# Kernel tuning notes

Hardware: AMD Instinct MI355X
Metric: run time of the kernel (lower is better)

Reference implementation:

```python
import jax, jax.numpy as jnp
import numpy as np

B, S, D, H = 64, 512, 256, 512

def setup_inputs() -> dict:
    key = jax.random.key(0)
    ks = jax.random.split(key, 16)
    s_in = 1.0 / np.sqrt(D)
    s_h = 1.0 / np.sqrt(H)
    inp = {
        "inputs": jax.random.normal(ks[0], (B, S, D), jnp.float32),
        # input-side gate weights (stored [D,H], equiv to torch Linear weight.T)
        "Wf": jax.random.uniform(ks[1], (D, H), jnp.float32, -s_in, s_in),
        "Wi": jax.random.uniform(ks[2], (D, H), jnp.float32, -s_in, s_in),
        "Wo": jax.random.uniform(ks[3], (D, H), jnp.float32, -s_in, s_in),
        "Wc": jax.random.uniform(ks[4], (D, H), jnp.float32, -s_in, s_in),
        "bf": jax.random.uniform(ks[5], (H,), jnp.float32, -s_in, s_in),
        "bi": jax.random.uniform(ks[6], (H,), jnp.float32, -s_in, s_in),
        "bo": jax.random.uniform(ks[7], (H,), jnp.float32, -s_in, s_in),
        "bc": jax.random.uniform(ks[8], (H,), jnp.float32, -s_in, s_in),
        # recurrent weights (bias=False)
        "Uf": jax.random.uniform(ks[9], (H, H), jnp.float32, -s_h, s_h),
        "Ui": jax.random.uniform(ks[10], (H, H), jnp.float32, -s_h, s_h),
        "Uo": jax.random.uniform(ks[11], (H, H), jnp.float32, -s_h, s_h),
        "Uc": jax.random.uniform(ks[12], (H, H), jnp.float32, -s_h, s_h),
        # output head
        "Wfc": jax.random.uniform(ks[13], (H, 1), jnp.float32, -s_h, s_h),
        "bfc": jax.random.uniform(ks[14], (1,), jnp.float32, -s_h, s_h),
    }
    return inp


def reference(inputs, Wf, Wi, Wo, Wc, bf, bi, bo, bc, Uf, Ui, Uo, Uc, Wfc, bfc):
    # Precompute all input-side gate projections in one big GEMM: [B,S,4H]
    Wx = jnp.concatenate([Wf, Wi, Wo, Wc], axis=1)            # [D,4H]
    bx = jnp.concatenate([bf, bi, bo, bc], axis=0)            # [4H]
    gx = jnp.einsum('bsd,dg->bsg', inputs, Wx) + bx           # [B,S,4H]
    Uh = jnp.concatenate([Uf, Ui, Uo, Uc], axis=1)            # [H,4H]

    h0 = jnp.zeros((inputs.shape[0], Uf.shape[0]), inputs.dtype)
    c0 = jnp.zeros_like(h0)
    Hd = Uf.shape[0]

    def step(carry, gx_t):
        h, c = carry
        g = gx_t + h @ Uh                                     # [B,4H]
        f_t = jax.nn.sigmoid(g[:, 0 * Hd:1 * Hd])
        i_t = jax.nn.sigmoid(g[:, 1 * Hd:2 * Hd])
        o_t = jax.nn.sigmoid(g[:, 2 * Hd:3 * Hd])
        chat = jnp.tanh(g[:, 3 * Hd:4 * Hd])
        c = f_t * c + i_t * chat
        h = o_t * jnp.tanh(c)
        return (h, c), h

    (h_t, c_t), hs = jax.lax.scan(step, (h0, c0), jnp.swapaxes(gx, 0, 1))
    outputs = jnp.swapaxes(hs, 0, 1)                          # [B,S,H]
    predictions = jnp.einsum('bsh,ho->bso', outputs, Wfc) + bfc
    return predictions, h_t, c_t
```

## Files before the change

### kernel.cpp

```cpp
#include <hip/hip_runtime.h>
#include <hip/hip_bf16.h>

#define B_ 64
#define S_ 512
#define D_ 256
#define H_ 512

typedef __attribute__((ext_vector_type(8))) short bf16x8;
typedef __attribute__((ext_vector_type(4))) float f32x4;
typedef __attribute__((ext_vector_type(4))) unsigned int uint4v;
typedef unsigned short ushort_t;

__device__ __forceinline__ ushort_t f2bf(float f) {
    __hip_bfloat16 h = __float2bfloat16(f);
    return *reinterpret_cast<ushort_t*>(&h);
}
__device__ __forceinline__ float sigmoid_f(float x) { return 1.f / (1.f + __expf(-x)); }
__device__ __forceinline__ float tanh_f(float x) { return 1.f - 2.f / (__expf(2.f * x) + 1.f); }

__device__ __forceinline__ void lds_barrier() {
    asm volatile("s_waitcnt lgkmcnt(0)\n\ts_barrier" ::: "memory");
}

__global__ __launch_bounds__(512, 2) void lstm_rec(
    const float* __restrict__ X,
    const float* __restrict__ Wf, const float* __restrict__ Wi,
    const float* __restrict__ Wo, const float* __restrict__ Wc,
    const float* __restrict__ bfp, const float* __restrict__ bip,
    const float* __restrict__ bop, const float* __restrict__ bcp,
    const float* __restrict__ Uf, const float* __restrict__ Ui,
    const float* __restrict__ Uo, const float* __restrict__ Uc,
    const float* __restrict__ Wfc,
    float* __restrict__ pred, unsigned int* __restrict__ hbufU,
    unsigned int* __restrict__ flags, unsigned int* __restrict__ xcdtab,
    float* __restrict__ outH, float* __restrict__ outC)
{
    __shared__ ushort_t hS[16 * 520];
    __shared__ ushort_t xS[16 * 264];
    __shared__ float gact[4][16][68];
    __shared__ int meta[2];

    const int tid  = threadIdx.x;
    const int w    = tid >> 6;
    const int lane = tid & 63;
    const int q    = lane >> 4;
    const int m    = lane & 15;
    const int gate = w >> 1;
    const int half = w & 1;

    if (w == 0) {
        unsigned int xcd;
        asm volatile("s_getreg_b32 %0, hwreg(HW_REG_XCC_ID)" : "=s"(xcd));
        xcd &= 15u;
        if (lane == 0)
            __hip_atomic_store(&xcdtab[blockIdx.x], xcd + 1u,
                               __ATOMIC_RELEASE, __HIP_MEMORY_SCOPE_AGENT);
        unsigned int entry;
        for (;;) {
            entry = __hip_atomic_load(&xcdtab[lane], __ATOMIC_ACQUIRE, __HIP_MEMORY_SCOPE_AGENT);
            if (__ballot(entry != 0u) == ~0ull) break;
            __builtin_amdgcn_s_sleep(1);
        }
        const unsigned int xcd_j = entry - 1u;
        const unsigned int key_j = (xcd_j << 8) | (unsigned int)lane;
        const unsigned int mykey = (xcd << 8) | (unsigned int)blockIdx.x;
        const int rank = __popcll(__ballot(key_j < mykey));
        const int c_lt = __popcll(__ballot(xcd_j < xcd));
        const int c_eq = __popcll(__ballot(xcd_j == xcd));
        const int gg   = rank >> 3;
        const bool uni = (c_lt <= gg * 8) && (gg * 8 + 8 <= c_lt + c_eq);
        if (lane == 0) { meta[0] = rank; meta[1] = uni ? 1 : 0; }
    }
    __syncthreads();
    const int  rank    = meta[0];
    const bool uniform = meta[1] != 0;
    if (rank >= 32) return;
    const int g = rank >> 3;
    const int s = rank & 7;

    const int ncol0 = s * 64 + half * 32 + m;
    const int ncol1 = ncol0 + 16;

    const float* Ug = (gate == 0) ? Uf : (gate == 1) ? Ui : (gate == 2) ? Uo : Uc;
    const float* Wg = (gate == 0) ? Wf : (gate == 1) ? Wi : (gate == 2) ? Wo : Wc;
    const float* bg = (gate == 0) ? bfp : (gate == 1) ? bip : (gate == 2) ? bop : bcp;

    const float bias0 = bg[ncol0];
    const float bias1 = bg[ncol1];

    bf16x8 UF[2][16];
    bf16x8 WF[2][8];
    #pragma unroll
    for (int tt = 0; tt < 2; ++tt) {
        const int nc = tt ? ncol1 : ncol0;
        #pragma unroll
        for (int ks = 0; ks < 16; ++ks) {
            bf16x8 v;
            #pragma unroll
            for (int j = 0; j < 8; ++j)
                v[j] = (short)f2bf(Ug[(ks * 32 + q * 8 + j) * H_ + nc]);
            UF[tt][ks] = v;
        }
        #pragma unroll
        for (int ks = 0; ks < 8; ++ks) {
            bf16x8 v;
            #pragma unroll
            for (int j = 0; j < 8; ++j)
                v[j] = (short)f2bf(Wg[(ks * 32 + q * 8 + j) * H_ + nc]);
            WF[tt][ks] = v;
        }
    }

    const int urow  = tid >> 5;
    const int upair = tid & 31;
    const float2 wfc2 = *(const float2*)&Wfc[s * 64 + 2 * upair];

    float cr0 = 0.f, cr1 = 0.f;

    unsigned int* flagsG = flags + g * 64;
    const int myflag = s * 8 + w;

    {
        const float* xsrc = &X[((size_t)(g * 16 + urow) * S_ + 0) * D_ + upair * 8];
        float4 a = *(const float4*)xsrc;
        float4 b = *(const float4*)(xsrc + 4);
        bf16x8 v;
        v[0] = (short)f2bf(a.x); v[1] = (short)f2bf(a.y);
        v[2] = (short)f2bf(a.z); v[3] = (short)f2bf(a.w);
        v[4] = (short)f2bf(b.x); v[5] = (short)f2bf(b.y);
        v[6] = (short)f2bf(b.z); v[7] = (short)f2bf(b.w);
        *(bf16x8*)&xS[urow * 264 + upair * 8] = v;
    }

    float4 xr0, xr1;

    for (int t = 0; t < S_; ++t) {
        if (t > 0) {
            const unsigned int tgt = (unsigned int)t;
            for (;;) {
                unsigned int f = __hip_atomic_load(&flagsG[lane],
                                                   __ATOMIC_RELAXED, __HIP_MEMORY_SCOPE_AGENT);
                if (__ballot(f >= tgt) == ~0ull) break;
                __builtin_amdgcn_s_sleep(1);
            }
        }

        {
            const int row  = tid >> 5;
            const int dcol = (tid & 31) * 8;
            const unsigned int* p0 = &hbufU[(size_t)((t % 3) * B_ + g * 16 + row) * 256 + dcol];
            const unsigned int* p1 = p0 + 4;
            uint4v ra, rb;
            if (uniform) {
                asm volatile(
                    "global_load_dwordx4 %0, %2, off sc0\n\t"
                    "global_load_dwordx4 %1, %3, off sc0\n\t"
                    "s_waitcnt vmcnt(0)"
                    : "=v"(ra), "=v"(rb) : "v"(p0), "v"(p1) : "memory");
            } else {
                asm volatile(
                    "global_load_dwordx4 %0, %2, off sc0 sc1\n\t"
                    "global_load_dwordx4 %1, %3, off sc0 sc1\n\t"
                    "s_waitcnt vmcnt(0)"
                    : "=v"(ra), "=v"(rb) : "v"(p0), "v"(p1) : "memory");
            }
            *(uint4v*)&hS[row * 520 + dcol * 2]     = ra;
            *(uint4v*)&hS[row * 520 + dcol * 2 + 8] = rb;
        }
        if (t + 1 < S_) {
            const float* xsrc = &X[((size_t)(g * 16 + urow) * S_ + (t + 1)) * D_ + upair * 8];
            xr0 = *(const float4*)xsrc;
            xr1 = *(const float4*)(xsrc + 4);
        }
        lds_barrier();

        f32x4 accA0 = {bias0, bias0, bias0, bias0};
        f32x4 accA1 = {bias1, bias1, bias1, bias1};
        f32x4 accB0 = {0.f, 0.f, 0.f, 0.f};
        f32x4 accB1 = {0.f, 0.f, 0.f, 0.f};
        #pragma unroll
        for (int ks = 0; ks < 8; ++ks) {
            bf16x8 a = *(const bf16x8*)&xS[m * 264 + ks * 32 + q * 8];
            accA0 = __builtin_amdgcn_mfma_f32_16x16x32_bf16(a, WF[0][ks], accA0, 0, 0, 0);
            accA1 = __builtin_amdgcn_mfma_f32_16x16x32_bf16(a, WF[1][ks], accA1, 0, 0, 0);
        }
        #pragma unroll
        for (int ks = 0; ks < 16; ++ks) {
            bf16x8 a = *(const bf16x8*)&hS[m * 520 + ks * 32 + q * 8];
            accB0 = __builtin_amdgcn_mfma_f32_16x16x32_bf16(a, UF[0][ks], accB0, 0, 0, 0);
            accB1 = __builtin_amdgcn_mfma_f32_16x16x32_bf16(a, UF[1][ks], accB1, 0, 0, 0);
        }
        #pragma unroll
        for (int j = 0; j < 4; ++j) {
            float v0 = accA0[j] + accB0[j];
            float v1 = accA1[j] + accB1[j];
            v0 = (gate < 3) ? sigmoid_f(v0) : tanh_f(v0);
            v1 = (gate < 3) ? sigmoid_f(v1) : tanh_f(v1);
            gact[gate][q * 4 + j][half * 32 + m]      = v0;
            gact[gate][q * 4 + j][half * 32 + 16 + m] = v1;
        }
        lds_barrier();

        float2 f2v = *(const float2*)&gact[0][urow][2 * upair];
        float2 i2v = *(const float2*)&gact[1][urow][2 * upair];
        float2 o2v = *(const float2*)&gact[2][urow][2 * upair];
        float2 ch2 = *(const float2*)&gact[3][urow][2 * upair];
        cr0 = f2v.x * cr0 + i2v.x * ch2.x;
        cr1 = f2v.y * cr1 + i2v.y * ch2.y;
        float hv0 = o2v.x * tanh_f(cr0);
        float hv1 = o2v.y * tanh_f(cr1);

        float pv = hv0 * wfc2.x + hv1 * wfc2.y;

        if (t < S_ - 1) {
            unsigned int packed = (unsigned int)f2bf(hv0) | ((unsigned int)f2bf(hv1) << 16);
            unsigned int* hdst =
                &hbufU[(size_t)(((t + 1) % 3) * B_ + g * 16 + urow) * 256 + s * 32 + upair];
            if (uniform) {
                asm volatile("global_store_dword %0, %1, off sc0" :: "v"(hdst), "v"(packed) : "memory");
            } else {
                asm volatile("global_store_dword %0, %1, off sc0 sc1" :: "v"(hdst), "v"(packed) : "memory");
            }
            bf16x8 v;
            v[0] = (short)f2bf(xr0.x); v[1] = (short)f2bf(xr0.y);
            v[2] = (short)f2bf(xr0.z); v[3] = (short)f2bf(xr0.w);
            v[4] = (short)f2bf(xr1.x); v[5] = (short)f2bf(xr1.y);
            v[6] = (short)f2bf(xr1.z); v[7] = (short)f2bf(xr1.w);
            *(bf16x8*)&xS[urow * 264 + upair * 8] = v;

            asm volatile("s_waitcnt vmcnt(0)" ::: "memory");
            if (lane == 0) {
                __hip_atomic_store(&flagsG[myflag], (unsigned int)(t + 1),
                                   __ATOMIC_RELAXED, __HIP_MEMORY_SCOPE_AGENT);
            }
        } else {
            *(float2*)&outH[(g * 16 + urow) * H_ + s * 64 + 2 * upair] = make_float2(hv0, hv1);
            *(float2*)&outC[(g * 16 + urow) * H_ + s * 64 + 2 * upair] = make_float2(cr0, cr1);
        }

        pv += __shfl_xor(pv, 16);
        pv += __shfl_xor(pv, 8);
        pv += __shfl_xor(pv, 4);
        pv += __shfl_xor(pv, 2);
        pv += __shfl_xor(pv, 1);
        if (upair == 0) atomicAdd(&pred[(g * 16 + urow) * S_ + t], pv);
    }
}

__global__ void pred_fin(const float* __restrict__ pred,
                         const float* __restrict__ bfc,
                         float* __restrict__ out)
{
    int i = blockIdx.x * blockDim.x + threadIdx.x;
    if (i < B_ * S_) out[i] = pred[i] + bfc[0];
}

extern "C" void kernel_launch(void* const* d_in, const int* in_sizes, int n_in,
                              void* d_out, int out_size, void* d_ws, size_t ws_size,
                              hipStream_t stream) {
    const float* X   = (const float*)d_in[0];
    const float* Wf  = (const float*)d_in[1];
    const float* Wi  = (const float*)d_in[2];
    const float* Wo  = (const float*)d_in[3];
    const float* Wc  = (const float*)d_in[4];
    const float* bfp = (const float*)d_in[5];
    const float* bip = (const float*)d_in[6];
    const float* bop = (const float*)d_in[7];
    const float* bcp = (const float*)d_in[8];
    const float* Uf  = (const float*)d_in[9];
    const float* Ui  = (const float*)d_in[10];
    const float* Uo  = (const float*)d_in[11];
    const float* Uc  = (const float*)d_in[12];
    const float* Wfc = (const float*)d_in[13];
    const float* bfc = (const float*)d_in[14];

    float*        pred   = (float*)d_ws;
    unsigned int* hbufU  = (unsigned int*)((char*)d_ws + 131072);
    unsigned int* flags  = (unsigned int*)((char*)d_ws + 327680);
    unsigned int* xcdtab = (unsigned int*)((char*)d_ws + 328704);

    hipMemsetAsync(d_ws, 0, 328704 + 256, stream);

    float* out = (float*)d_out;
    lstm_rec<<<64, 512, 0, stream>>>(X, Wf, Wi, Wo, Wc, bfp, bip, bop, bcp,
                                     Uf, Ui, Uo, Uc, Wfc,
                                     pred, hbufU, flags, xcdtab,
                                     out + 32768, out + 65536);
    pred_fin<<<128, 256, 0, stream>>>(pred, bfc, out);
}
```

Before: 2.281 ms.

## Replace flag-based step sync with step-tagged 64-bit hidden-state entries

Each hidden-state element is now stored as a 64-bit word holding the bf16 pair plus the step number, written with one atomic store. Consumers spin directly on the data until every tag matches, which removes the separate flag array, the wait-for-stores fence and the flag polling round trip. The XCD-aware rank assignment is dropped and blocks map directly from blockIdx with only 32 blocks launched, and the ring buffer shrinks from three slots to two. In exchange the h-exchange traffic doubles, all loads use device-scope coherence with no XCD-local fast path, and the spin loop no longer sleeps.

```diff
diff --git a/kernel.cpp b/kernel.cpp
--- a/kernel.cpp
+++ b/kernel.cpp
@@ -10,6 +10,7 @@
 typedef __attribute__((ext_vector_type(4))) float f32x4;
 typedef __attribute__((ext_vector_type(4))) unsigned int uint4v;
 typedef unsigned short ushort_t;
+typedef unsigned long long u64_t;
 
 __device__ __forceinline__ ushort_t f2bf(float f) {
     __hip_bfloat16 h = __float2bfloat16(f);
@@ -31,14 +32,12 @@
     const float* __restrict__ Uf, const float* __restrict__ Ui,
     const float* __restrict__ Uo, const float* __restrict__ Uc,
     const float* __restrict__ Wfc,
-    float* __restrict__ pred, unsigned int* __restrict__ hbufU,
-    unsigned int* __restrict__ flags, unsigned int* __restrict__ xcdtab,
+    float* __restrict__ pred, u64_t* __restrict__ hbuf,
     float* __restrict__ outH, float* __restrict__ outC)
 {
     __shared__ ushort_t hS[16 * 520];
     __shared__ ushort_t xS[16 * 264];
     __shared__ float gact[4][16][68];
-    __shared__ int meta[2];
 
     const int tid  = threadIdx.x;
     const int w    = tid >> 6;
@@ -48,35 +47,8 @@
     const int gate = w >> 1;
     const int half = w & 1;
 
-    if (w == 0) {
-        unsigned int xcd;
-        asm volatile("s_getreg_b32 %0, hwreg(HW_REG_XCC_ID)" : "=s"(xcd));
-        xcd &= 15u;
-        if (lane == 0)
-            __hip_atomic_store(&xcdtab[blockIdx.x], xcd + 1u,
-                               __ATOMIC_RELEASE, __HIP_MEMORY_SCOPE_AGENT);
-        unsigned int entry;
-        for (;;) {
-            entry = __hip_atomic_load(&xcdtab[lane], __ATOMIC_ACQUIRE, __HIP_MEMORY_SCOPE_AGENT);
-            if (__ballot(entry != 0u) == ~0ull) break;
-            __builtin_amdgcn_s_sleep(1);
-        }
-        const unsigned int xcd_j = entry - 1u;
-        const unsigned int key_j = (xcd_j << 8) | (unsigned int)lane;
-        const unsigned int mykey = (xcd << 8) | (unsigned int)blockIdx.x;
-        const int rank = __popcll(__ballot(key_j < mykey));
-        const int c_lt = __popcll(__ballot(xcd_j < xcd));
-        const int c_eq = __popcll(__ballot(xcd_j == xcd));
-        const int gg   = rank >> 3;
-        const bool uni = (c_lt <= gg * 8) && (gg * 8 + 8 <= c_lt + c_eq);
-        if (lane == 0) { meta[0] = rank; meta[1] = uni ? 1 : 0; }
-    }
-    __syncthreads();
-    const int  rank    = meta[0];
-    const bool uniform = meta[1] != 0;
-    if (rank >= 32) return;
-    const int g = rank >> 3;
-    const int s = rank & 7;
+    const int g = blockIdx.x >> 3;
+    const int s = blockIdx.x & 7;
 
     const int ncol0 = s * 64 + half * 32 + m;
     const int ncol1 = ncol0 + 16;
@@ -116,9 +88,6 @@
     const float2 wfc2 = *(const float2*)&Wfc[s * 64 + 2 * upair];
 
     float cr0 = 0.f, cr1 = 0.f;
-
-    unsigned int* flagsG = flags + g * 64;
-    const int myflag = s * 8 + w;
 
     {
         const float* xsrc = &X[((size_t)(g * 16 + urow) * S_ + 0) * D_ + upair * 8];
@@ -135,42 +104,38 @@
     float4 xr0, xr1;
 
     for (int t = 0; t < S_; ++t) {
-        if (t > 0) {
-            const unsigned int tgt = (unsigned int)t;
+        {
+            const int pr = upair * 8;
+            u64_t* pe = hbuf + ((size_t)((t & 1) * B_ + g * 16 + urow) * 256 + pr);
+            const unsigned int tg = (unsigned int)t;
+            u64_t e0, e1, e2, e3, e4, e5, e6, e7;
             for (;;) {
-                unsigned int f = __hip_atomic_load(&flagsG[lane],
-                                                   __ATOMIC_RELAXED, __HIP_MEMORY_SCOPE_AGENT);
-                if (__ballot(f >= tgt) == ~0ull) break;
-                __builtin_amdgcn_s_sleep(1);
+                e0 = __hip_atomic_load(pe + 0, __ATOMIC_RELAXED, __HIP_MEMORY_SCOPE_AGENT);
+                e1 = __hip_atomic_load(pe + 1, __ATOMIC_RELAXED, __HIP_MEMORY_SCOPE_AGENT);
+                e2 = __hip_atomic_load(pe + 2, __ATOMIC_RELAXED, __HIP_MEMORY_SCOPE_AGENT);
+                e3 = __hip_atomic_load(pe + 3, __ATOMIC_RELAXED, __HIP_MEMORY_SCOPE_AGENT);
+                e4 = __hip_atomic_load(pe + 4, __ATOMIC_RELAXED, __HIP_MEMORY_SCOPE_AGENT);
+                e5 = __hip_atomic_load(pe + 5, __ATOMIC_RELAXED, __HIP_MEMORY_SCOPE_AGENT);
+                e6 = __hip_atomic_load(pe + 6, __ATOMIC_RELAXED, __HIP_MEMORY_SCOPE_AGENT);
+                e7 = __hip_atomic_load(pe + 7, __ATOMIC_RELAXED, __HIP_MEMORY_SCOPE_AGENT);
+                bool ok = (unsigned int)(e0 >> 32) == tg && (unsigned int)(e1 >> 32) == tg
+                       && (unsigned int)(e2 >> 32) == tg && (unsigned int)(e3 >> 32) == tg
+                       && (unsigned int)(e4 >> 32) == tg && (unsigned int)(e5 >> 32) == tg
+                       && (unsigned int)(e6 >> 32) == tg && (unsigned int)(e7 >> 32) == tg;
+                if (__ballot(ok) == ~0ull) break;
             }
-        }
-
-        {
-            const int row  = tid >> 5;
-            const int dcol = (tid & 31) * 8;
-            const unsigned int* p0 = &hbufU[(size_t)((t % 3) * B_ + g * 16 + row) * 256 + dcol];
-            const unsigned int* p1 = p0 + 4;
+            if (t + 1 < S_) {
+                const float* xsrc = &X[((size_t)(g * 16 + urow) * S_ + (t + 1)) * D_ + upair * 8];
+                xr0 = *(const float4*)xsrc;
+                xr1 = *(const float4*)(xsrc + 4);
+            }
             uint4v ra, rb;
-            if (uniform) {
-                asm volatile(
-                    "global_load_dwordx4 %0, %2, off sc0\n\t"
-                    "global_load_dwordx4 %1, %3, off sc0\n\t"
-                    "s_waitcnt vmcnt(0)"
-                    : "=v"(ra), "=v"(rb) : "v"(p0), "v"(p1) : "memory");
-            } else {
-                asm volatile(
-                    "global_load_dwordx4 %0, %2, off sc0 sc1\n\t"
-                    "global_load_dwordx4 %1, %3, off sc0 sc1\n\t"
-                    "s_waitcnt vmcnt(0)"
-                    : "=v"(ra), "=v"(rb) : "v"(p0), "v"(p1) : "memory");
-            }
-            *(uint4v*)&hS[row * 520 + dcol * 2]     = ra;
-            *(uint4v*)&hS[row * 520 + dcol * 2 + 8] = rb;
-        }
-        if (t + 1 < S_) {
-            const float* xsrc = &X[((size_t)(g * 16 + urow) * S_ + (t + 1)) * D_ + upair * 8];
-            xr0 = *(const float4*)xsrc;
-            xr1 = *(const float4*)(xsrc + 4);
+            ra[0] = (unsigned int)e0; ra[1] = (unsigned int)e1;
+            ra[2] = (unsigned int)e2; ra[3] = (unsigned int)e3;
+            rb[0] = (unsigned int)e4; rb[1] = (unsigned int)e5;
+            rb[2] = (unsigned int)e6; rb[3] = (unsigned int)e7;
+            *(uint4v*)&hS[urow * 520 + pr * 2]     = ra;
+            *(uint4v*)&hS[urow * 520 + pr * 2 + 8] = rb;
         }
         lds_barrier();
 
@@ -210,34 +175,24 @@
         float hv0 = o2v.x * tanh_f(cr0);
         float hv1 = o2v.y * tanh_f(cr1);
 
-        float pv = hv0 * wfc2.x + hv1 * wfc2.y;
-
         if (t < S_ - 1) {
             unsigned int packed = (unsigned int)f2bf(hv0) | ((unsigned int)f2bf(hv1) << 16);
-            unsigned int* hdst =
-                &hbufU[(size_t)(((t + 1) % 3) * B_ + g * 16 + urow) * 256 + s * 32 + upair];
-            if (uniform) {
-                asm volatile("global_store_dword %0, %1, off sc0" :: "v"(hdst), "v"(packed) : "memory");
-            } else {
-                asm volatile("global_store_dword %0, %1, off sc0 sc1" :: "v"(hdst), "v"(packed) : "memory");
-            }
+            u64_t ent = ((u64_t)(unsigned int)(t + 1) << 32) | (u64_t)packed;
+            u64_t* hdst = hbuf + ((size_t)(((t + 1) & 1) * B_ + g * 16 + urow) * 256
+                                  + s * 32 + upair);
+            __hip_atomic_store(hdst, ent, __ATOMIC_RELAXED, __HIP_MEMORY_SCOPE_AGENT);
             bf16x8 v;
             v[0] = (short)f2bf(xr0.x); v[1] = (short)f2bf(xr0.y);
             v[2] = (short)f2bf(xr0.z); v[3] = (short)f2bf(xr0.w);
             v[4] = (short)f2bf(xr1.x); v[5] = (short)f2bf(xr1.y);
             v[6] = (short)f2bf(xr1.z); v[7] = (short)f2bf(xr1.w);
             *(bf16x8*)&xS[urow * 264 + upair * 8] = v;
-
-            asm volatile("s_waitcnt vmcnt(0)" ::: "memory");
-            if (lane == 0) {
-                __hip_atomic_store(&flagsG[myflag], (unsigned int)(t + 1),
-                                   __ATOMIC_RELAXED, __HIP_MEMORY_SCOPE_AGENT);
-            }
         } else {
             *(float2*)&outH[(g * 16 + urow) * H_ + s * 64 + 2 * upair] = make_float2(hv0, hv1);
             *(float2*)&outC[(g * 16 + urow) * H_ + s * 64 + 2 * upair] = make_float2(cr0, cr1);
         }
 
+        float pv = hv0 * wfc2.x + hv1 * wfc2.y;
         pv += __shfl_xor(pv, 16);
         pv += __shfl_xor(pv, 8);
         pv += __shfl_xor(pv, 4);
@@ -274,17 +229,15 @@
     const float* Wfc = (const float*)d_in[13];
     const float* bfc = (const float*)d_in[14];
 
-    float*        pred   = (float*)d_ws;
-    unsigned int* hbufU  = (unsigned int*)((char*)d_ws + 131072);
-    unsigned int* flags  = (unsigned int*)((char*)d_ws + 327680);
-    unsigned int* xcdtab = (unsigned int*)((char*)d_ws + 328704);
-
-    hipMemsetAsync(d_ws, 0, 328704 + 256, stream);
+    float*        pred = (float*)d_ws;
+    u64_t*        hbuf = (u64_t*)((char*)d_ws + 131072);
+
+    hipMemsetAsync(d_ws, 0, 131072 + 262144, stream);
 
     float* out = (float*)d_out;
-    lstm_rec<<<64, 512, 0, stream>>>(X, Wf, Wi, Wo, Wc, bfp, bip, bop, bcp,
+    lstm_rec<<<32, 512, 0, stream>>>(X, Wf, Wi, Wo, Wc, bfp, bip, bop, bcp,
                                      Uf, Ui, Uo, Uc, Wfc,
-                                     pred, hbufU, flags, xcdtab,
+                                     pred, hbuf,
                                      out + 32768, out + 65536);
     pred_fin<<<128, 256, 0, stream>>>(pred, bfc, out);
 }
```

Result: slower. 2.828 ms (+24.0%).

## Replace flag-based sync with step-tagged hidden-state entries polled directly

Applied to the files above, without the earlier changes.

Each hidden-state value is now stored as a 64-bit entry that pairs the packed bf16 pair with its timestep tag. Consumers poll the data itself until every tag matches, which removes the separate flag array, the vmcnt wait before the flag store and one global round trip per step. The ring shrinks from three slots to two, since the tag tells stale data apart. In exchange, each step reads twice as many bytes, and correctness depends on the 64-bit store and load being atomic.

```diff
diff --git a/kernel.cpp b/kernel.cpp
--- a/kernel.cpp
+++ b/kernel.cpp
@@ -10,6 +10,7 @@
 typedef __attribute__((ext_vector_type(4))) float f32x4;
 typedef __attribute__((ext_vector_type(4))) unsigned int uint4v;
 typedef unsigned short ushort_t;
+typedef unsigned long long u64_t;
 
 __device__ __forceinline__ ushort_t f2bf(float f) {
     __hip_bfloat16 h = __float2bfloat16(f);
@@ -31,8 +32,8 @@
     const float* __restrict__ Uf, const float* __restrict__ Ui,
     const float* __restrict__ Uo, const float* __restrict__ Uc,
     const float* __restrict__ Wfc,
-    float* __restrict__ pred, unsigned int* __restrict__ hbufU,
-    unsigned int* __restrict__ flags, unsigned int* __restrict__ xcdtab,
+    float* __restrict__ pred, u64_t* __restrict__ hbuf,
+    unsigned int* __restrict__ xcdtab,
     float* __restrict__ outH, float* __restrict__ outC)
 {
     __shared__ ushort_t hS[16 * 520];
@@ -117,9 +118,6 @@
 
     float cr0 = 0.f, cr1 = 0.f;
 
-    unsigned int* flagsG = flags + g * 64;
-    const int myflag = s * 8 + w;
-
     {
         const float* xsrc = &X[((size_t)(g * 16 + urow) * S_ + 0) * D_ + upair * 8];
         float4 a = *(const float4*)xsrc;
@@ -135,42 +133,63 @@
     float4 xr0, xr1;
 
     for (int t = 0; t < S_; ++t) {
-        if (t > 0) {
-            const unsigned int tgt = (unsigned int)t;
-            for (;;) {
-                unsigned int f = __hip_atomic_load(&flagsG[lane],
-                                                   __ATOMIC_RELAXED, __HIP_MEMORY_SCOPE_AGENT);
-                if (__ballot(f >= tgt) == ~0ull) break;
-                __builtin_amdgcn_s_sleep(1);
+        {
+            const int row = tid >> 5;
+            const int pr  = (tid & 31) * 8;
+            u64_t* pe = hbuf + ((size_t)((t & 1) * B_ + g * 16 + row) * 256 + pr);
+            const unsigned int tg = (unsigned int)t;
+            uint4v ra, rb;
+            bool got = false;
+            if (uniform) {
+                uint4v r0, r1, r2, r3;
+                asm volatile(
+                    "global_load_dwordx4 %0, %4, off sc0\n\t"
+                    "global_load_dwordx4 %1, %5, off sc0\n\t"
+                    "global_load_dwordx4 %2, %6, off sc0\n\t"
+                    "global_load_dwordx4 %3, %7, off sc0\n\t"
+                    "s_waitcnt vmcnt(0)"
+                    : "=v"(r0), "=v"(r1), "=v"(r2), "=v"(r3)
+                    : "v"(pe), "v"(pe + 2), "v"(pe + 4), "v"(pe + 6)
+                    : "memory");
+                bool ok = r0[1] == tg && r0[3] == tg && r1[1] == tg && r1[3] == tg
+                       && r2[1] == tg && r2[3] == tg && r3[1] == tg && r3[3] == tg;
+                if (__ballot(ok) == ~0ull) {
+                    ra[0] = r0[0]; ra[1] = r0[2]; ra[2] = r1[0]; ra[3] = r1[2];
+                    rb[0] = r2[0]; rb[1] = r2[2]; rb[2] = r3[0]; rb[3] = r3[2];
+                    got = true;
+                }
             }
-        }
-
-        {
-            const int row  = tid >> 5;
-            const int dcol = (tid & 31) * 8;
-            const unsigned int* p0 = &hbufU[(size_t)((t % 3) * B_ + g * 16 + row) * 256 + dcol];
-            const unsigned int* p1 = p0 + 4;
-            uint4v ra, rb;
-            if (uniform) {
-                asm volatile(
-                    "global_load_dwordx4 %0, %2, off sc0\n\t"
-                    "global_load_dwordx4 %1, %3, off sc0\n\t"
-                    "s_waitcnt vmcnt(0)"
-                    : "=v"(ra), "=v"(rb) : "v"(p0), "v"(p1) : "memory");
-            } else {
-                asm volatile(
-                    "global_load_dwordx4 %0, %2, off sc0 sc1\n\t"
-                    "global_load_dwordx4 %1, %3, off sc0 sc1\n\t"
-                    "s_waitcnt vmcnt(0)"
-                    : "=v"(ra), "=v"(rb) : "v"(p0), "v"(p1) : "memory");
+            if (!got) {
+                for (;;) {
+                    u64_t e0 = __hip_atomic_load(pe + 0, __ATOMIC_RELAXED, __HIP_MEMORY_SCOPE_AGENT);
+                    u64_t e1 = __hip_atomic_load(pe + 1, __ATOMIC_RELAXED, __HIP_MEMORY_SCOPE_AGENT);
+                    u64_t e2 = __hip_atomic_load(pe + 2, __ATOMIC_RELAXED, __HIP_MEMORY_SCOPE_AGENT);
+                    u64_t e3 = __hip_atomic_load(pe + 3, __ATOMIC_RELAXED, __HIP_MEMORY_SCOPE_AGENT);
+                    u64_t e4 = __hip_atomic_load(pe + 4, __ATOMIC_RELAXED, __HIP_MEMORY_SCOPE_AGENT);
+                    u64_t e5 = __hip_atomic_load(pe + 5, __ATOMIC_RELAXED, __HIP_MEMORY_SCOPE_AGENT);
+                    u64_t e6 = __hip_atomic_load(pe + 6, __ATOMIC_RELAXED, __HIP_MEMORY_SCOPE_AGENT);
+                    u64_t e7 = __hip_atomic_load(pe + 7, __ATOMIC_RELAXED, __HIP_MEMORY_SCOPE_AGENT);
+                    bool ok = (unsigned int)(e0 >> 32) == tg && (unsigned int)(e1 >> 32) == tg
+                           && (unsigned int)(e2 >> 32) == tg && (unsigned int)(e3 >> 32) == tg
+                           && (unsigned int)(e4 >> 32) == tg && (unsigned int)(e5 >> 32) == tg
+                           && (unsigned int)(e6 >> 32) == tg && (unsigned int)(e7 >> 32) == tg;
+                    if (__ballot(ok) == ~0ull) {
+                        ra[0] = (unsigned int)e0; ra[1] = (unsigned int)e1;
+                        ra[2] = (unsigned int)e2; ra[3] = (unsigned int)e3;
+                        rb[0] = (unsigned int)e4; rb[1] = (unsigned int)e5;
+                        rb[2] = (unsigned int)e6; rb[3] = (unsigned int)e7;
+                        break;
+                    }
+                    __builtin_amdgcn_s_sleep(1);
+                }
             }
-            *(uint4v*)&hS[row * 520 + dcol * 2]     = ra;
-            *(uint4v*)&hS[row * 520 + dcol * 2 + 8] = rb;
-        }
-        if (t + 1 < S_) {
-            const float* xsrc = &X[((size_t)(g * 16 + urow) * S_ + (t + 1)) * D_ + upair * 8];
-            xr0 = *(const float4*)xsrc;
-            xr1 = *(const float4*)(xsrc + 4);
+            if (t + 1 < S_) {
+                const float* xsrc = &X[((size_t)(g * 16 + urow) * S_ + (t + 1)) * D_ + upair * 8];
+                xr0 = *(const float4*)xsrc;
+                xr1 = *(const float4*)(xsrc + 4);
+            }
+            *(uint4v*)&hS[row * 520 + pr * 2]     = ra;
+            *(uint4v*)&hS[row * 520 + pr * 2 + 8] = rb;
         }
         lds_barrier();
 
@@ -210,34 +229,25 @@
         float hv0 = o2v.x * tanh_f(cr0);
         float hv1 = o2v.y * tanh_f(cr1);
 
-        float pv = hv0 * wfc2.x + hv1 * wfc2.y;
-
         if (t < S_ - 1) {
             unsigned int packed = (unsigned int)f2bf(hv0) | ((unsigned int)f2bf(hv1) << 16);
-            unsigned int* hdst =
-                &hbufU[(size_t)(((t + 1) % 3) * B_ + g * 16 + urow) * 256 + s * 32 + upair];
-            if (uniform) {
-                asm volatile("global_store_dword %0, %1, off sc0" :: "v"(hdst), "v"(packed) : "memory");
-            } else {
-                asm volatile("global_store_dword %0, %1, off sc0 sc1" :: "v"(hdst), "v"(packed) : "memory");
-            }
+            u64_t ent = ((u64_t)(unsigned int)(t + 1) << 32) | (u64_t)packed;
+            u64_t* hdst = hbuf + ((size_t)(((t + 1) & 1) * B_ + g * 16 + urow) * 256
+                                  + s * 32 + upair);
+            asm volatile("global_store_dwordx2 %0, %1, off sc0 sc1"
+                         :: "v"(hdst), "v"(ent) : "memory");
             bf16x8 v;
             v[0] = (short)f2bf(xr0.x); v[1] = (short)f2bf(xr0.y);
             v[2] = (short)f2bf(xr0.z); v[3] = (short)f2bf(xr0.w);
             v[4] = (short)f2bf(xr1.x); v[5] = (short)f2bf(xr1.y);
             v[6] = (short)f2bf(xr1.z); v[7] = (short)f2bf(xr1.w);
             *(bf16x8*)&xS[urow * 264 + upair * 8] = v;
-
-            asm volatile("s_waitcnt vmcnt(0)" ::: "memory");
-            if (lane == 0) {
-                __hip_atomic_store(&flagsG[myflag], (unsigned int)(t + 1),
-                                   __ATOMIC_RELAXED, __HIP_MEMORY_SCOPE_AGENT);
-            }
         } else {
             *(float2*)&outH[(g * 16 + urow) * H_ + s * 64 + 2 * upair] = make_float2(hv0, hv1);
             *(float2*)&outC[(g * 16 + urow) * H_ + s * 64 + 2 * upair] = make_float2(cr0, cr1);
         }
 
+        float pv = hv0 * wfc2.x + hv1 * wfc2.y;
         pv += __shfl_xor(pv, 16);
         pv += __shfl_xor(pv, 8);
         pv += __shfl_xor(pv, 4);
@@ -275,16 +285,15 @@
     const float* bfc = (const float*)d_in[14];
 
     float*        pred   = (float*)d_ws;
-    unsigned int* hbufU  = (unsigned int*)((char*)d_ws + 131072);
-    unsigned int* flags  = (unsigned int*)((char*)d_ws + 327680);
-    unsigned int* xcdtab = (unsigned int*)((char*)d_ws + 328704);
-
-    hipMemsetAsync(d_ws, 0, 328704 + 256, stream);
+    u64_t*        hbuf   = (u64_t*)((char*)d_ws + 131072);
+    unsigned int* xcdtab = (unsigned int*)((char*)d_ws + 393216);
+
+    hipMemsetAsync(d_ws, 0, 393216 + 256, stream);
 
     float* out = (float*)d_out;
     lstm_rec<<<64, 512, 0, stream>>>(X, Wf, Wi, Wo, Wc, bfp, bip, bop, bcp,
                                      Uf, Ui, Uo, Uc, Wfc,
-                                     pred, hbufU, flags, xcdtab,
+                                     pred, hbuf, xcdtab,
                                      out + 32768, out + 65536);
     pred_fin<<<128, 256, 0, stream>>>(pred, bfc, out);
 }
```

Result: faster. 2.231 ms (-2.2%).

## Poll step flags via L2 atomics with padded slots and overlap input GEMM

Applied to the files above, without the earlier changes.

Flags are padded to 128-byte slots so each one sits on its own cache line. When all blocks share an XCD, the flags are written with an atomic swap and polled with an atomic add of zero, so the poll resolves at L2 instead of through a system-coherent load. A plain-store copy of each flag is kept as a fallback path in case the atomic poll stalls. The input-projection MFMAs now run before the wait, so that compute overlaps with flag polling. Only wave 0 polls, behind extra barriers, and the launch-bounds occupancy hint is dropped; this adds complexity and risks some extra barrier cost.

```diff
diff --git a/kernel.cpp b/kernel.cpp
--- a/kernel.cpp
+++ b/kernel.cpp
@@ -22,7 +22,7 @@
     asm volatile("s_waitcnt lgkmcnt(0)\n\ts_barrier" ::: "memory");
 }
 
-__global__ __launch_bounds__(512, 2) void lstm_rec(
+__global__ __launch_bounds__(512) void lstm_rec(
     const float* __restrict__ X,
     const float* __restrict__ Wf, const float* __restrict__ Wi,
     const float* __restrict__ Wo, const float* __restrict__ Wc,
@@ -117,8 +117,9 @@
 
     float cr0 = 0.f, cr1 = 0.f;
 
-    unsigned int* flagsG = flags + g * 64;
+    unsigned int* flagsG = flags + g * 64 * 32;
     const int myflag = s * 8 + w;
+    bool rmw_ok = true;
 
     {
         const float* xsrc = &X[((size_t)(g * 16 + urow) * S_ + 0) * D_ + upair * 8];
@@ -135,15 +136,65 @@
     float4 xr0, xr1;
 
     for (int t = 0; t < S_; ++t) {
-        if (t > 0) {
-            const unsigned int tgt = (unsigned int)t;
-            for (;;) {
-                unsigned int f = __hip_atomic_load(&flagsG[lane],
+        lds_barrier();
+
+        const unsigned int tgt = (unsigned int)t;
+        const bool doPoll = (t > 0);
+        unsigned int fv1 = 0;
+
+        if (doPoll && w == 0 && uniform && rmw_ok) {
+            asm volatile("global_atomic_add %0, %1, %2, off sc0"
+                         : "=v"(fv1) : "v"(&flagsG[lane * 32]), "v"(0u) : "memory");
+        }
+
+        f32x4 accA0 = {bias0, bias0, bias0, bias0};
+        f32x4 accA1 = {bias1, bias1, bias1, bias1};
+        #pragma unroll
+        for (int ks = 0; ks < 8; ++ks) {
+            bf16x8 a = *(const bf16x8*)&xS[m * 264 + ks * 32 + q * 8];
+            accA0 = __builtin_amdgcn_mfma_f32_16x16x32_bf16(a, WF[0][ks], accA0, 0, 0, 0);
+            accA1 = __builtin_amdgcn_mfma_f32_16x16x32_bf16(a, WF[1][ks], accA1, 0, 0, 0);
+        }
+
+        if (doPoll && w == 0) {
+            if (uniform && rmw_ok) {
+                asm volatile("s_waitcnt vmcnt(0)" : "+v"(fv1) :: "memory");
+                __builtin_amdgcn_sched_barrier(0);
+                bool done = (__ballot(fv1 >= tgt) == ~0ull);
+                int rounds = 0;
+                while (!done && rounds < 16) {
+                    ++rounds;
+                    if (rounds > 2) __builtin_amdgcn_s_sleep(1);
+                    asm volatile("global_atomic_add %0, %1, %2, off sc0\n\t"
+                                 "s_waitcnt vmcnt(0)"
+                                 : "=v"(fv1) : "v"(&flagsG[lane * 32]), "v"(0u) : "memory");
+                    __builtin_amdgcn_sched_barrier(0);
+                    done = (__ballot(fv1 >= tgt) == ~0ull);
+                }
+                if (!done) {
+                    unsigned int fb = __hip_atomic_load(&flagsG[lane * 32 + 16],
+                                                        __ATOMIC_RELAXED, __HIP_MEMORY_SCOPE_AGENT);
+                    if (__ballot(fb >= tgt) == ~0ull) {
+                        rmw_ok = false;
+                    } else {
+                        for (;;) {
+                            __builtin_amdgcn_s_sleep(1);
+                            fb = __hip_atomic_load(&flagsG[lane * 32 + 16],
                                                    __ATOMIC_RELAXED, __HIP_MEMORY_SCOPE_AGENT);
-                if (__ballot(f >= tgt) == ~0ull) break;
-                __builtin_amdgcn_s_sleep(1);
+                            if (__ballot(fb >= tgt) == ~0ull) break;
+                        }
+                    }
+                }
+            } else {
+                for (;;) {
+                    unsigned int fb = __hip_atomic_load(&flagsG[lane * 32 + 16],
+                                                        __ATOMIC_RELAXED, __HIP_MEMORY_SCOPE_AGENT);
+                    if (__ballot(fb >= tgt) == ~0ull) break;
+                    __builtin_amdgcn_s_sleep(1);
+                }
             }
         }
+        lds_barrier();
 
         {
             const int row  = tid >> 5;
@@ -174,16 +225,8 @@
         }
         lds_barrier();
 
-        f32x4 accA0 = {bias0, bias0, bias0, bias0};
-        f32x4 accA1 = {bias1, bias1, bias1, bias1};
         f32x4 accB0 = {0.f, 0.f, 0.f, 0.f};
         f32x4 accB1 = {0.f, 0.f, 0.f, 0.f};
-        #pragma unroll
-        for (int ks = 0; ks < 8; ++ks) {
-            bf16x8 a = *(const bf16x8*)&xS[m * 264 + ks * 32 + q * 8];
-            accA0 = __builtin_amdgcn_mfma_f32_16x16x32_bf16(a, WF[0][ks], accA0, 0, 0, 0);
-            accA1 = __builtin_amdgcn_mfma_f32_16x16x32_bf16(a, WF[1][ks], accA1, 0, 0, 0);
-        }
         #pragma unroll
         for (int ks = 0; ks < 16; ++ks) {
             bf16x8 a = *(const bf16x8*)&hS[m * 520 + ks * 32 + q * 8];
@@ -230,8 +273,17 @@
 
             asm volatile("s_waitcnt vmcnt(0)" ::: "memory");
             if (lane == 0) {
-                __hip_atomic_store(&flagsG[myflag], (unsigned int)(t + 1),
-                                   __ATOMIC_RELAXED, __HIP_MEMORY_SCOPE_AGENT);
+                unsigned int tv = (unsigned int)(t + 1);
+                unsigned int* fpA = &flagsG[myflag * 32];
+                unsigned int* fpB = fpA + 16;
+                if (uniform) {
+                    asm volatile("global_atomic_swap %0, %1, off"
+                                 :: "v"(fpA), "v"(tv) : "memory");
+                    asm volatile("global_store_dword %0, %1, off sc0 sc1"
+                                 :: "v"(fpB), "v"(tv) : "memory");
+                } else {
+                    __hip_atomic_store(fpB, tv, __ATOMIC_RELAXED, __HIP_MEMORY_SCOPE_AGENT);
+                }
             }
         } else {
             *(float2*)&outH[(g * 16 + urow) * H_ + s * 64 + 2 * upair] = make_float2(hv0, hv1);
@@ -277,9 +329,9 @@
     float*        pred   = (float*)d_ws;
     unsigned int* hbufU  = (unsigned int*)((char*)d_ws + 131072);
     unsigned int* flags  = (unsigned int*)((char*)d_ws + 327680);
-    unsigned int* xcdtab = (unsigned int*)((char*)d_ws + 328704);
-
-    hipMemsetAsync(d_ws, 0, 328704 + 256, stream);
+    unsigned int* xcdtab = (unsigned int*)((char*)d_ws + 360448);
+
+    hipMemsetAsync(d_ws, 0, 360704, stream);
 
     float* out = (float*)d_out;
     lstm_rec<<<64, 512, 0, stream>>>(X, Wf, Wi, Wo, Wc, bfp, bip, bop, bcp,
```

New measurement: 2.933 ms. +28.6%, slower.
